# Optimization experiments

Hardware: AMD Instinct MI355X
Metric: run time of the kernel (lower is better)

## Reference

```python
import jax, jax.numpy as jnp
import numpy as np

B, S, K, H = 512, 128, 4, 128  # batch, seq_len, interest_num, hidden_size
ROUTING_TIMES = 3
EPS = 1e-9


def setup_inputs() -> dict:
    key = jax.random.key(0)
    k1, k2 = jax.random.split(key)
    item_eb = jax.random.normal(k1, (B, S, H), dtype=jnp.float32)
    mask = jnp.ones((B, S), dtype=jnp.float32)
    # learned bilinear map parameter (bilinear_type == 2)
    w = jax.random.normal(k2, (1, S, K * H, H), dtype=jnp.float32) * 0.02
    return {"item_eb": item_eb, "mask": mask, "w": w}


def _squash(cap):
    # cap: [B, K, 1, H]
    n = jnp.sum(cap * cap, axis=-1, keepdims=True)
    return (n / (1.0 + n) / jnp.sqrt(n + EPS)) * cap


def reference(item_eb, mask, w):
    # bilinear_type==2: sum(w[:, :S] * item_eb[:, :, None, :], axis=3)
    # expressed as an einsum to avoid the [B,S,K*H,H] intermediate
    item_eb_hat = jnp.einsum('bsh,sdh->bsd', item_eb, w[0])          # [B, S, K*H]
    item_eb_hat = item_eb_hat.reshape(B, S, K, H).transpose(0, 2, 1, 3)  # [B, K, S, H]
    hat_iter = jax.lax.stop_gradient(item_eb_hat)  # stop_grad=True

    atten_mask = jnp.broadcast_to(mask[:, None, :], (B, K, S))
    capsule_weight = jnp.zeros((B, K, S), dtype=item_eb.dtype)  # bilinear_type > 0

    interest_capsule = None
    for i in range(ROUTING_TIMES):
        # torch F.softmax with implicit dim on a 3D tensor -> dim=0 (legacy)
        sw = jax.nn.softmax(capsule_weight, axis=0)
        sw = jnp.where(atten_mask == 0, 0.0, sw)[:, :, None, :]  # [B, K, 1, S]
        src = hat_iter if i < 2 else item_eb_hat
        interest_capsule = _squash(jnp.matmul(sw, src))  # [B, K, 1, H]
        if i < 2:
            delta = jnp.matmul(hat_iter, interest_capsule.transpose(0, 1, 3, 2))  # [B,K,S,1]
            capsule_weight = capsule_weight + delta.reshape(B, K, S)

    return interest_capsule.reshape(B, K, H)
```

## Files before the change

### kernel.cpp

```cpp
#include <hip/hip_runtime.h>
#include <math.h>

#define BB 512
#define SS 128
#define KK 4
#define HH 128
#define DD 512

typedef __attribute__((ext_vector_type(8))) short bf16x8;
typedef __attribute__((ext_vector_type(4))) float f32x4;

__device__ __forceinline__ unsigned short f2bf(float f) {
  unsigned u = __float_as_uint(f);
  unsigned r = u + 0x7fffu + ((u >> 16) & 1u);
  return (unsigned short)(r >> 16);
}
__device__ __forceinline__ float bfhi(unsigned u) { return __uint_as_float(u & 0xffff0000u); }
__device__ __forceinline__ float bflo(unsigned u) { return __uint_as_float(u << 16); }
__device__ __forceinline__ unsigned pk2(float a, float b) {
  return (unsigned)f2bf(a) | ((unsigned)f2bf(b) << 16);
}

__global__ __launch_bounds__(256) void einsum_mfma(
    const float* __restrict__ A,
    const float* __restrict__ W,
    unsigned short* __restrict__ hat)
{
  __shared__ unsigned short Al[128 * 64];
  __shared__ unsigned short Wl[128 * 64];
  const int s  = blockIdx.z;
  const int b0 = blockIdx.x * 128;
  const int dt = blockIdx.y;
  const int d0 = dt * 128;
  const int t  = threadIdx.x;
  const int lane = t & 63, wv = t >> 6;
  const int qm = wv & 1, qn = wv >> 1;
  const int n16 = lane & 15, kq = lane >> 4;
  const int r = t >> 1, cq = t & 1;

  f32x4 acc[4][4] = {};

  for (int ks = 0; ks < 128; ks += 64) {
    const float* ga = A + ((size_t)(b0 + r) * SS + s) * HH + ks + cq * 32;
    const float* gw = W + ((size_t)s * DD + d0 + r) * HH + ks + cq * 32;
    #pragma unroll
    for (int j = 0; j < 4; j++) {
      float4 a0 = *(const float4*)(ga + 8 * j);
      float4 a1 = *(const float4*)(ga + 8 * j + 4);
      float4 w0 = *(const float4*)(gw + 8 * j);
      float4 w1 = *(const float4*)(gw + 8 * j + 4);
      const int goff = ((cq * 4 + j + r) & 7) * 8;
      uint4 pa, pw;
      pa.x = pk2(a0.x, a0.y); pa.y = pk2(a0.z, a0.w);
      pa.z = pk2(a1.x, a1.y); pa.w = pk2(a1.z, a1.w);
      pw.x = pk2(w0.x, w0.y); pw.y = pk2(w0.z, w0.w);
      pw.z = pk2(w1.x, w1.y); pw.w = pk2(w1.z, w1.w);
      *(uint4*)&Al[r * 64 + goff] = pa;
      *(uint4*)&Wl[r * 64 + goff] = pw;
    }
    __syncthreads();
    #pragma unroll
    for (int kk = 0; kk < 2; kk++) {
      bf16x8 af[4], bfr[4];
      #pragma unroll
      for (int i = 0; i < 4; i++) {
        const int ra = qm * 64 + i * 16 + n16;
        const int rb = qn * 64 + i * 16 + n16;
        af[i]  = *(const bf16x8*)&Wl[ra * 64 + ((kk * 4 + kq + ra) & 7) * 8];
        bfr[i] = *(const bf16x8*)&Al[rb * 64 + ((kk * 4 + kq + rb) & 7) * 8];
      }
      #pragma unroll
      for (int i = 0; i < 4; i++)
        #pragma unroll
        for (int j = 0; j < 4; j++)
          acc[i][j] = __builtin_amdgcn_mfma_f32_16x16x32_bf16(af[i], bfr[j], acc[i][j], 0, 0, 0);
    }
    __syncthreads();
  }

  #pragma unroll
  for (int j = 0; j < 4; j++) {
    const int b = b0 + qn * 64 + j * 16 + n16;
    unsigned short* orow = hat + (((size_t)b * KK + dt) * SS + s) * HH;
    #pragma unroll
    for (int i = 0; i < 4; i++) {
      const int h = qm * 64 + i * 16 + kq * 4;
      ushort4 o;
      o.x = f2bf(acc[i][j][0]); o.y = f2bf(acc[i][j][1]);
      o.z = f2bf(acc[i][j][2]); o.w = f2bf(acc[i][j][3]);
      *(ushort4*)(orow + h) = o;
    }
  }
}

__global__ __launch_bounds__(256) void softmax_k(
    const float* __restrict__ cw, const float* __restrict__ mask,
    float* __restrict__ sw)
{
  __shared__ float rbuf[4];
  const int s = blockIdx.x, k = blockIdx.y, t = threadIdx.x;
  const size_t base = ((size_t)k * SS + s) * BB;
  float v0 = cw[base + t], v1 = cw[base + 256 + t];
  float m = fmaxf(v0, v1);
  #pragma unroll
  for (int o = 32; o; o >>= 1) m = fmaxf(m, __shfl_xor(m, o));
  if ((t & 63) == 0) rbuf[t >> 6] = m;
  __syncthreads();
  m = fmaxf(fmaxf(rbuf[0], rbuf[1]), fmaxf(rbuf[2], rbuf[3]));
  float e0 = expf(v0 - m), e1 = expf(v1 - m);
  float ssum = e0 + e1;
  #pragma unroll
  for (int o = 32; o; o >>= 1) ssum += __shfl_xor(ssum, o);
  __syncthreads();
  if ((t & 63) == 0) rbuf[t >> 6] = ssum;
  __syncthreads();
  float inv = 1.f / (rbuf[0] + rbuf[1] + rbuf[2] + rbuf[3]);
  float m0 = mask[(size_t)t * SS + s];
  float m1 = mask[(size_t)(t + 256) * SS + s];
  sw[base + t]       = (m0 == 0.f) ? 0.f : e0 * inv;
  sw[base + 256 + t] = (m1 == 0.f) ? 0.f : e1 * inv;
}

__global__ __launch_bounds__(256) void routing_k(
    const unsigned short* __restrict__ hat, const float* __restrict__ mask,
    const float* __restrict__ sw_in, float* __restrict__ cw,
    float* __restrict__ out, int mode)
{
  __shared__ float sw_l[128];
  __shared__ float4 red4[8][33];
  __shared__ float cq_l[128];
  const int b = blockIdx.x, k = blockIdx.y, t = threadIdx.x;

  if (t < 128) {
    if (mode == 0) {
      sw_l[t] = (mask[(size_t)b * SS + t] == 0.f) ? 0.f : (1.f / 512.f);
    } else {
      sw_l[t] = sw_in[((size_t)k * SS + t) * BB + b];
    }
  }
  __syncthreads();

  const unsigned short* hrow = hat + ((size_t)b * KK + k) * SS * HH;

  {
    const int h4 = t & 31, sg = t >> 5;
    const uint2* hp = (const uint2*)hrow;
    float4 a = make_float4(0.f, 0.f, 0.f, 0.f);
    #pragma unroll 4
    for (int i = 0; i < 16; i++) {
      int s = sg * 16 + i;
      uint2 v = hp[s * 32 + h4];
      float wv = sw_l[s];
      a.x = fmaf(wv, bflo(v.x), a.x);
      a.y = fmaf(wv, bfhi(v.x), a.y);
      a.z = fmaf(wv, bflo(v.y), a.z);
      a.w = fmaf(wv, bfhi(v.y), a.w);
    }
    red4[sg][h4] = a;
  }
  __syncthreads();

  if (t < 32) {
    float4 cap = red4[0][t];
    #pragma unroll
    for (int sg = 1; sg < 8; sg++) {
      float4 r = red4[sg][t];
      cap.x += r.x; cap.y += r.y; cap.z += r.z; cap.w += r.w;
    }
    float sq = cap.x * cap.x + cap.y * cap.y + cap.z * cap.z + cap.w * cap.w;
    #pragma unroll
    for (int o = 16; o; o >>= 1) sq += __shfl_xor(sq, o);
    const float n = sq;
    const float fac = n / (1.f + n) / sqrtf(n + 1e-9f);
    cap.x *= fac; cap.y *= fac; cap.z *= fac; cap.w *= fac;
    ((float4*)cq_l)[t] = cap;
    if (mode == 2)
      ((float4*)(out + ((size_t)b * KK + k) * HH))[t] = cap;
  }
  __syncthreads();

  if (mode < 2) {
    const int s = t >> 1, hh = t & 1;
    const uint4* hp16 = (const uint4*)hrow;
    float d = 0.f;
    #pragma unroll
    for (int j = 0; j < 8; j++) {
      uint4 v = hp16[s * 16 + hh * 8 + j];
      const float* cq = cq_l + hh * 64 + j * 8;
      d += bflo(v.x) * cq[0] + bfhi(v.x) * cq[1]
         + bflo(v.y) * cq[2] + bfhi(v.y) * cq[3]
         + bflo(v.z) * cq[4] + bfhi(v.z) * cq[5]
         + bflo(v.w) * cq[6] + bfhi(v.w) * cq[7];
    }
    d += __shfl_xor(d, 1);
    if (hh == 0) {
      float* p = cw + ((size_t)k * SS + s) * BB + b;
      if (mode == 0) *p = d; else *p += d;
    }
  }
}

extern "C" void kernel_launch(void* const* d_in, const int* in_sizes, int n_in,
                              void* d_out, int out_size, void* d_ws, size_t ws_size,
                              hipStream_t stream) {
  const float* item_eb = (const float*)d_in[0];
  const float* mask    = (const float*)d_in[1];
  const float* w       = (const float*)d_in[2];
  float* out = (float*)d_out;

  char* ws = (char*)d_ws;
  unsigned short* hat_bf = (unsigned short*)ws;
  float* cw  = (float*)(ws + 67108864);
  float* swb = (float*)(ws + 68157440);

  einsum_mfma<<<dim3(4, 4, 128), 256, 0, stream>>>(item_eb, w, hat_bf);

  routing_k<<<dim3(BB, KK), 256, 0, stream>>>(hat_bf, mask, nullptr, cw, out, 0);
  softmax_k<<<dim3(SS, KK), 256, 0, stream>>>(cw, mask, swb);
  routing_k<<<dim3(BB, KK), 256, 0, stream>>>(hat_bf, mask, swb, cw, out, 1);
  softmax_k<<<dim3(SS, KK), 256, 0, stream>>>(cw, mask, swb);
  routing_k<<<dim3(BB, KK), 256, 0, stream>>>(hat_bf, mask, swb, cw, out, 2);
}
```

Measured before the change: 209.1 us.

## Pre-convert inputs to bf16 in a prep kernel and stage hat rows in LDS

Adds a prep kernel that converts item_eb to bf16 in an s-major layout and converts w to bf16, so the einsum loads bf16 tiles directly without converting in the inner loop. The einsum grid is reordered so that blocks sharing the same s launch next to each other. routing_k now loads the whole hat row for a (b,k) into padded LDS once and reuses it for both the weighted sum and the delta dot product, instead of reading it from global memory twice. The cost is an extra kernel and an extra round trip of about 34 MB through global memory for the converted copies.

```diff
diff --git a/kernel.cpp b/kernel.cpp
--- a/kernel.cpp
+++ b/kernel.cpp
@@ -17,46 +17,64 @@
 }
 __device__ __forceinline__ float bfhi(unsigned u) { return __uint_as_float(u & 0xffff0000u); }
 __device__ __forceinline__ float bflo(unsigned u) { return __uint_as_float(u << 16); }
-__device__ __forceinline__ unsigned pk2(float a, float b) {
-  return (unsigned)f2bf(a) | ((unsigned)f2bf(b) << 16);
+
+__global__ __launch_bounds__(256) void prep_k(
+    const float* __restrict__ item, const float* __restrict__ w,
+    unsigned short* __restrict__ item_t, unsigned short* __restrict__ w_bf)
+{
+  const int blk = blockIdx.x, t = threadIdx.x;
+  if (blk < 8192) {
+    const int rid = blk * 8 + (t >> 5);
+    const int b = rid >> 7, s = rid & 127;
+    const int c = t & 31;
+    float4 v = ((const float4*)(item + (size_t)rid * HH))[c];
+    ushort4 o;
+    o.x = f2bf(v.x); o.y = f2bf(v.y); o.z = f2bf(v.z); o.w = f2bf(v.w);
+    ((ushort4*)(item_t + ((size_t)s * BB + b) * HH))[c] = o;
+  } else {
+    size_t base = (size_t)(blk - 8192) * 2048 + t;
+    const float4* src = (const float4*)w;
+    ushort4* dst = (ushort4*)w_bf;
+    #pragma unroll
+    for (int j = 0; j < 8; j++) {
+      float4 v = src[base + 256 * j];
+      ushort4 o;
+      o.x = f2bf(v.x); o.y = f2bf(v.y); o.z = f2bf(v.z); o.w = f2bf(v.w);
+      dst[base + 256 * j] = o;
+    }
+  }
 }
 
 __global__ __launch_bounds__(256) void einsum_mfma(
-    const float* __restrict__ A,
-    const float* __restrict__ W,
+    const unsigned short* __restrict__ At,
+    const unsigned short* __restrict__ W,
     unsigned short* __restrict__ hat)
 {
   __shared__ unsigned short Al[128 * 64];
   __shared__ unsigned short Wl[128 * 64];
-  const int s  = blockIdx.z;
-  const int b0 = blockIdx.x * 128;
-  const int dt = blockIdx.y;
+  const int s  = blockIdx.x;
+  const int b0 = (blockIdx.y & 3) * 128;
+  const int dt = blockIdx.y >> 2;
   const int d0 = dt * 128;
   const int t  = threadIdx.x;
   const int lane = t & 63, wv = t >> 6;
   const int qm = wv & 1, qn = wv >> 1;
   const int n16 = lane & 15, kq = lane >> 4;
-  const int r = t >> 1, cq = t & 1;
+  const int sr = t >> 3, sc = t & 7;
+
+  const unsigned short* Abase = At + ((size_t)s * BB + b0) * HH;
+  const unsigned short* Wbase = W + ((size_t)s * DD + d0) * HH;
 
   f32x4 acc[4][4] = {};
-
   for (int ks = 0; ks < 128; ks += 64) {
-    const float* ga = A + ((size_t)(b0 + r) * SS + s) * HH + ks + cq * 32;
-    const float* gw = W + ((size_t)s * DD + d0 + r) * HH + ks + cq * 32;
     #pragma unroll
     for (int j = 0; j < 4; j++) {
-      float4 a0 = *(const float4*)(ga + 8 * j);
-      float4 a1 = *(const float4*)(ga + 8 * j + 4);
-      float4 w0 = *(const float4*)(gw + 8 * j);
-      float4 w1 = *(const float4*)(gw + 8 * j + 4);
-      const int goff = ((cq * 4 + j + r) & 7) * 8;
-      uint4 pa, pw;
-      pa.x = pk2(a0.x, a0.y); pa.y = pk2(a0.z, a0.w);
-      pa.z = pk2(a1.x, a1.y); pa.w = pk2(a1.z, a1.w);
-      pw.x = pk2(w0.x, w0.y); pw.y = pk2(w0.z, w0.w);
-      pw.z = pk2(w1.x, w1.y); pw.w = pk2(w1.z, w1.w);
-      *(uint4*)&Al[r * 64 + goff] = pa;
-      *(uint4*)&Wl[r * 64 + goff] = pw;
+      const int r = sr + 32 * j;
+      uint4 va = *(const uint4*)(Abase + (size_t)r * HH + ks + sc * 8);
+      uint4 vw = *(const uint4*)(Wbase + (size_t)r * HH + ks + sc * 8);
+      const int goff = ((sc + r) & 7) * 8;
+      *(uint4*)&Al[r * 64 + goff] = va;
+      *(uint4*)&Wl[r * 64 + goff] = vw;
     }
     __syncthreads();
     #pragma unroll
@@ -126,30 +144,33 @@
     const float* __restrict__ sw_in, float* __restrict__ cw,
     float* __restrict__ out, int mode)
 {
+  __shared__ unsigned short hat_l[128 * 136];
   __shared__ float sw_l[128];
-  __shared__ float4 red4[8][33];
-  __shared__ float cq_l[128];
+  __shared__ float4 red4[8][32];
+  __shared__ float4 cq4[32];
   const int b = blockIdx.x, k = blockIdx.y, t = threadIdx.x;
 
   if (t < 128) {
-    if (mode == 0) {
-      sw_l[t] = (mask[(size_t)b * SS + t] == 0.f) ? 0.f : (1.f / 512.f);
-    } else {
-      sw_l[t] = sw_in[((size_t)k * SS + t) * BB + b];
-    }
-  }
-  __syncthreads();
-
-  const unsigned short* hrow = hat + ((size_t)b * KK + k) * SS * HH;
+    sw_l[t] = (mode == 0)
+      ? ((mask[(size_t)b * SS + t] == 0.f) ? 0.f : (1.f / 512.f))
+      : sw_in[((size_t)k * SS + t) * BB + b];
+  }
+  const uint4* hp = (const uint4*)(hat + ((size_t)b * KK + k) * SS * HH);
+  #pragma unroll
+  for (int j = 0; j < 8; j++) {
+    const int f = t + 256 * j;
+    const int s = f >> 4, c = f & 15;
+    *(uint4*)&hat_l[s * 136 + c * 8] = hp[f];
+  }
+  __syncthreads();
 
   {
     const int h4 = t & 31, sg = t >> 5;
-    const uint2* hp = (const uint2*)hrow;
     float4 a = make_float4(0.f, 0.f, 0.f, 0.f);
     #pragma unroll 4
     for (int i = 0; i < 16; i++) {
-      int s = sg * 16 + i;
-      uint2 v = hp[s * 32 + h4];
+      const int s = sg * 16 + i;
+      uint2 v = *(const uint2*)&hat_l[s * 136 + h4 * 4];
       float wv = sw_l[s];
       a.x = fmaf(wv, bflo(v.x), a.x);
       a.y = fmaf(wv, bfhi(v.x), a.y);
@@ -173,7 +194,7 @@
     const float n = sq;
     const float fac = n / (1.f + n) / sqrtf(n + 1e-9f);
     cap.x *= fac; cap.y *= fac; cap.z *= fac; cap.w *= fac;
-    ((float4*)cq_l)[t] = cap;
+    cq4[t] = cap;
     if (mode == 2)
       ((float4*)(out + ((size_t)b * KK + k) * HH))[t] = cap;
   }
@@ -181,16 +202,17 @@
 
   if (mode < 2) {
     const int s = t >> 1, hh = t & 1;
-    const uint4* hp16 = (const uint4*)hrow;
+    const uint4* row = (const uint4*)&hat_l[s * 136 + hh * 64];
     float d = 0.f;
     #pragma unroll
     for (int j = 0; j < 8; j++) {
-      uint4 v = hp16[s * 16 + hh * 8 + j];
-      const float* cq = cq_l + hh * 64 + j * 8;
-      d += bflo(v.x) * cq[0] + bfhi(v.x) * cq[1]
-         + bflo(v.y) * cq[2] + bfhi(v.y) * cq[3]
-         + bflo(v.z) * cq[4] + bfhi(v.z) * cq[5]
-         + bflo(v.w) * cq[6] + bfhi(v.w) * cq[7];
+      uint4 v = row[j];
+      float4 qa = cq4[hh * 16 + 2 * j];
+      float4 qb = cq4[hh * 16 + 2 * j + 1];
+      d += bflo(v.x) * qa.x + bfhi(v.x) * qa.y
+         + bflo(v.y) * qa.z + bfhi(v.y) * qa.w
+         + bflo(v.z) * qb.x + bfhi(v.z) * qb.y
+         + bflo(v.w) * qb.z + bfhi(v.w) * qb.w;
     }
     d += __shfl_xor(d, 1);
     if (hh == 0) {
@@ -209,11 +231,14 @@
   float* out = (float*)d_out;
 
   char* ws = (char*)d_ws;
-  unsigned short* hat_bf = (unsigned short*)ws;
-  float* cw  = (float*)(ws + 67108864);
-  float* swb = (float*)(ws + 68157440);
-
-  einsum_mfma<<<dim3(4, 4, 128), 256, 0, stream>>>(item_eb, w, hat_bf);
+  unsigned short* hat_bf  = (unsigned short*)ws;
+  unsigned short* item_t  = (unsigned short*)(ws + 67108864);
+  unsigned short* w_bf    = (unsigned short*)(ws + 83886080);
+  float* cw  = (float*)(ws + 100663296);
+  float* swb = (float*)(ws + 101711872);
+
+  prep_k<<<dim3(9216), 256, 0, stream>>>(item_eb, w, item_t, w_bf);
+  einsum_mfma<<<dim3(128, 16), 256, 0, stream>>>(item_t, w_bf, hat_bf);
 
   routing_k<<<dim3(BB, KK), 256, 0, stream>>>(hat_bf, mask, nullptr, cw, out, 0);
   softmax_k<<<dim3(SS, KK), 256, 0, stream>>>(cw, mask, swb);
```

Result: faster. 184.6 us (-11.7%).

## Transpose capsule-weight layout, stage hat rows in LDS, remap einsum grid

Applied to the files above, without the earlier changes.

Capsule weights and softmax outputs move from a [K,S,B] layout to [B,K,S], so the routing kernel writes and reads them contiguously. The softmax kernel now tiles 32 sequence positions per block and transposes through shared memory, and mask application moves into the routing kernel. The routing kernel stages each 128x128 bf16 hat tile in padded LDS once instead of reading it from global twice. The einsum grid is also reordered so the sequence index is the fastest-varying block dimension, and softmax now runs on only 16 blocks, which could underuse the device.

```diff
diff --git a/kernel.cpp b/kernel.cpp
--- a/kernel.cpp
+++ b/kernel.cpp
@@ -28,9 +28,9 @@
 {
   __shared__ unsigned short Al[128 * 64];
   __shared__ unsigned short Wl[128 * 64];
-  const int s  = blockIdx.z;
-  const int b0 = blockIdx.x * 128;
-  const int dt = blockIdx.y;
+  const int s  = blockIdx.x;
+  const int b0 = (blockIdx.y & 3) * 128;
+  const int dt = blockIdx.y >> 2;
   const int d0 = dt * 128;
   const int t  = threadIdx.x;
   const int lane = t & 63, wv = t >> 6;
@@ -39,7 +39,6 @@
   const int r = t >> 1, cq = t & 1;
 
   f32x4 acc[4][4] = {};
-
   for (int ks = 0; ks < 128; ks += 64) {
     const float* ga = A + ((size_t)(b0 + r) * SS + s) * HH + ks + cq * 32;
     const float* gw = W + ((size_t)s * DD + d0 + r) * HH + ks + cq * 32;
@@ -94,31 +93,57 @@
 }
 
 __global__ __launch_bounds__(256) void softmax_k(
-    const float* __restrict__ cw, const float* __restrict__ mask,
-    float* __restrict__ sw)
+    const float* __restrict__ cw, float* __restrict__ sw)
 {
-  __shared__ float rbuf[4];
-  const int s = blockIdx.x, k = blockIdx.y, t = threadIdx.x;
-  const size_t base = ((size_t)k * SS + s) * BB;
-  float v0 = cw[base + t], v1 = cw[base + 256 + t];
-  float m = fmaxf(v0, v1);
-  #pragma unroll
-  for (int o = 32; o; o >>= 1) m = fmaxf(m, __shfl_xor(m, o));
-  if ((t & 63) == 0) rbuf[t >> 6] = m;
-  __syncthreads();
-  m = fmaxf(fmaxf(rbuf[0], rbuf[1]), fmaxf(rbuf[2], rbuf[3]));
-  float e0 = expf(v0 - m), e1 = expf(v1 - m);
-  float ssum = e0 + e1;
-  #pragma unroll
-  for (int o = 32; o; o >>= 1) ssum += __shfl_xor(ssum, o);
-  __syncthreads();
-  if ((t & 63) == 0) rbuf[t >> 6] = ssum;
-  __syncthreads();
-  float inv = 1.f / (rbuf[0] + rbuf[1] + rbuf[2] + rbuf[3]);
-  float m0 = mask[(size_t)t * SS + s];
-  float m1 = mask[(size_t)(t + 256) * SS + s];
-  sw[base + t]       = (m0 == 0.f) ? 0.f : e0 * inv;
-  sw[base + 256 + t] = (m1 == 0.f) ? 0.f : e1 * inv;
+  __shared__ float T[512 * 33];
+  __shared__ float red[2][8][32];
+  const int s0 = blockIdx.x * 32, k = blockIdx.y, t = threadIdx.x;
+  const int bg = t >> 3, c = t & 7;
+
+  #pragma unroll
+  for (int i = 0; i < 16; i++) {
+    const int b = i * 32 + bg;
+    float4 v = *(const float4*)(cw + ((size_t)b * KK + k) * SS + s0 + c * 4);
+    float* Tr = &T[b * 33 + c * 4];
+    Tr[0] = v.x; Tr[1] = v.y; Tr[2] = v.z; Tr[3] = v.w;
+  }
+  __syncthreads();
+
+  const int sc = t & 31, grp = t >> 5;
+  float mx = -3.4e38f;
+  #pragma unroll 8
+  for (int i = 0; i < 64; i++)
+    mx = fmaxf(mx, T[(grp * 64 + i) * 33 + sc]);
+  red[0][grp][sc] = mx;
+  __syncthreads();
+  float mall = red[0][0][sc];
+  #pragma unroll
+  for (int g = 1; g < 8; g++) mall = fmaxf(mall, red[0][g][sc]);
+  float sm = 0.f;
+  #pragma unroll 8
+  for (int i = 0; i < 64; i++) {
+    float* p = &T[(grp * 64 + i) * 33 + sc];
+    float e = __expf(*p - mall);
+    *p = e; sm += e;
+  }
+  red[1][grp][sc] = sm;
+  __syncthreads();
+  float tot = 0.f;
+  #pragma unroll
+  for (int g = 0; g < 8; g++) tot += red[1][g][sc];
+  const float inv = 1.f / tot;
+  #pragma unroll 8
+  for (int i = 0; i < 64; i++)
+    T[(grp * 64 + i) * 33 + sc] *= inv;
+  __syncthreads();
+
+  #pragma unroll
+  for (int i = 0; i < 16; i++) {
+    const int b = i * 32 + bg;
+    const float* Tr = &T[b * 33 + c * 4];
+    *(float4*)(sw + ((size_t)b * KK + k) * SS + s0 + c * 4) =
+        make_float4(Tr[0], Tr[1], Tr[2], Tr[3]);
+  }
 }
 
 __global__ __launch_bounds__(256) void routing_k(
@@ -126,30 +151,34 @@
     const float* __restrict__ sw_in, float* __restrict__ cw,
     float* __restrict__ out, int mode)
 {
+  __shared__ unsigned short hat_l[128 * 136];
   __shared__ float sw_l[128];
-  __shared__ float4 red4[8][33];
-  __shared__ float cq_l[128];
+  __shared__ float4 red4[8][32];
+  __shared__ float4 cq4[32];
   const int b = blockIdx.x, k = blockIdx.y, t = threadIdx.x;
 
   if (t < 128) {
-    if (mode == 0) {
-      sw_l[t] = (mask[(size_t)b * SS + t] == 0.f) ? 0.f : (1.f / 512.f);
-    } else {
-      sw_l[t] = sw_in[((size_t)k * SS + t) * BB + b];
-    }
-  }
-  __syncthreads();
-
-  const unsigned short* hrow = hat + ((size_t)b * KK + k) * SS * HH;
+    const float mk = mask[(size_t)b * SS + t];
+    sw_l[t] = (mode == 0)
+      ? ((mk == 0.f) ? 0.f : (1.f / 512.f))
+      : ((mk == 0.f) ? 0.f : sw_in[((size_t)b * KK + k) * SS + t]);
+  }
+  const uint4* hp = (const uint4*)(hat + ((size_t)b * KK + k) * SS * HH);
+  #pragma unroll
+  for (int j = 0; j < 8; j++) {
+    const int f = t + 256 * j;
+    const int s = f >> 4, c = f & 15;
+    *(uint4*)&hat_l[s * 136 + c * 8] = hp[f];
+  }
+  __syncthreads();
 
   {
     const int h4 = t & 31, sg = t >> 5;
-    const uint2* hp = (const uint2*)hrow;
     float4 a = make_float4(0.f, 0.f, 0.f, 0.f);
     #pragma unroll 4
     for (int i = 0; i < 16; i++) {
-      int s = sg * 16 + i;
-      uint2 v = hp[s * 32 + h4];
+      const int s = sg * 16 + i;
+      uint2 v = *(const uint2*)&hat_l[s * 136 + h4 * 4];
       float wv = sw_l[s];
       a.x = fmaf(wv, bflo(v.x), a.x);
       a.y = fmaf(wv, bfhi(v.x), a.y);
@@ -173,7 +202,7 @@
     const float n = sq;
     const float fac = n / (1.f + n) / sqrtf(n + 1e-9f);
     cap.x *= fac; cap.y *= fac; cap.z *= fac; cap.w *= fac;
-    ((float4*)cq_l)[t] = cap;
+    cq4[t] = cap;
     if (mode == 2)
       ((float4*)(out + ((size_t)b * KK + k) * HH))[t] = cap;
   }
@@ -181,20 +210,21 @@
 
   if (mode < 2) {
     const int s = t >> 1, hh = t & 1;
-    const uint4* hp16 = (const uint4*)hrow;
+    const uint4* row = (const uint4*)&hat_l[s * 136 + hh * 64];
     float d = 0.f;
     #pragma unroll
     for (int j = 0; j < 8; j++) {
-      uint4 v = hp16[s * 16 + hh * 8 + j];
-      const float* cq = cq_l + hh * 64 + j * 8;
-      d += bflo(v.x) * cq[0] + bfhi(v.x) * cq[1]
-         + bflo(v.y) * cq[2] + bfhi(v.y) * cq[3]
-         + bflo(v.z) * cq[4] + bfhi(v.z) * cq[5]
-         + bflo(v.w) * cq[6] + bfhi(v.w) * cq[7];
+      uint4 v = row[j];
+      float4 qa = cq4[hh * 16 + 2 * j];
+      float4 qb = cq4[hh * 16 + 2 * j + 1];
+      d += bflo(v.x) * qa.x + bfhi(v.x) * qa.y
+         + bflo(v.y) * qa.z + bfhi(v.y) * qa.w
+         + bflo(v.z) * qb.x + bfhi(v.z) * qb.y
+         + bflo(v.w) * qb.z + bfhi(v.w) * qb.w;
     }
     d += __shfl_xor(d, 1);
     if (hh == 0) {
-      float* p = cw + ((size_t)k * SS + s) * BB + b;
+      float* p = cw + ((size_t)b * KK + k) * SS + s;
       if (mode == 0) *p = d; else *p += d;
     }
   }
@@ -213,11 +243,11 @@
   float* cw  = (float*)(ws + 67108864);
   float* swb = (float*)(ws + 68157440);
 
-  einsum_mfma<<<dim3(4, 4, 128), 256, 0, stream>>>(item_eb, w, hat_bf);
+  einsum_mfma<<<dim3(128, 16), 256, 0, stream>>>(item_eb, w, hat_bf);
 
   routing_k<<<dim3(BB, KK), 256, 0, stream>>>(hat_bf, mask, nullptr, cw, out, 0);
-  softmax_k<<<dim3(SS, KK), 256, 0, stream>>>(cw, mask, swb);
+  softmax_k<<<dim3(4, KK), 256, 0, stream>>>(cw, swb);
   routing_k<<<dim3(BB, KK), 256, 0, stream>>>(hat_bf, mask, swb, cw, out, 1);
-  softmax_k<<<dim3(SS, KK), 256, 0, stream>>>(cw, mask, swb);
+  softmax_k<<<dim3(4, KK), 256, 0, stream>>>(cw, swb);
   routing_k<<<dim3(BB, KK), 256, 0, stream>>>(hat_bf, mask, swb, cw, out, 2);
 }
```

After: 196.2 us. -6.1%, faster.
